# Kernel tuning notes

Measured on AMD Instinct MI355X. Metric: run time of the kernel, lower is better.

The kernel has to match this reference:

```python
import jax, jax.numpy as jnp
from jax import lax
import numpy as np
import math

B, T, D = 4, 4096, 1024
K, H = 128, 8
KH = K // H
KER = 4
M = 4 * D  # mlp hidden


def _ln(x, g, b):
    m = jnp.mean(x, axis=-1, keepdims=True)
    v = jnp.var(x, axis=-1, keepdims=True)
    return (x - m) / jnp.sqrt(v + 1e-5) * g + b


def setup_inputs() -> dict:
    key = jax.random.key(0)
    ks = jax.random.split(key, 20)
    s = lambda i, shape, sc=0.02: jax.random.normal(ks[i], shape, dtype=jnp.float32) * sc
    inp = {}
    inp["x"] = jax.random.normal(ks[0], (B, T, D), dtype=jnp.float32)
    inp["prev_eig"] = jax.random.normal(ks[1], (B, T, 2 * K), dtype=jnp.float32)
    inp["in_proj_w"] = s(2, (2 * K, D))
    inp["conv_w"] = s(3, (2 * K, 1, KER), 0.3)          # depthwise Conv1d weight
    inp["conv_b"] = s(4, (2 * K,), 0.02)
    inp["mem_gate"] = jnp.float32(-3.0)
    inp["mem_proj_w"] = jnp.eye(2 * K, dtype=jnp.float32) + s(5, (2 * K, 2 * K), 0.02)
    # log_decay uniform in [center-1, center+0.5], center = -2 + 1.5*(1/5)
    center = -2.0 + 1.5 * (1.0 / 5.0)
    inp["log_decay"] = jax.random.uniform(ks[6], (K,), dtype=jnp.float32, minval=center - 1.0, maxval=center + 0.5)
    inp["frequency"] = jnp.linspace(0.0, 2.0 * math.pi * (1.0 - 1.0 / K), K, dtype=jnp.float32)
    inp["coupling"] = jnp.eye(KH, dtype=jnp.float32)[None] + 0.01 * jax.random.normal(ks[7], (H, KH, KH), dtype=jnp.float32) / math.sqrt(KH)
    inp["out_proj_w"] = s(8, (D, 2 * K))
    inp["gate_w"] = s(9, (D, D))
    inp["gate_b"] = jnp.full((D,), -2.0, dtype=jnp.float32)
    inp["mlp_w1"] = s(10, (M, D))
    inp["mlp_b1"] = jnp.zeros((M,), jnp.float32)
    inp["mlp_w2"] = s(11, (D, M))
    inp["mlp_b2"] = jnp.zeros((D,), jnp.float32)
    inp["n1_g"] = jnp.ones((D,), jnp.float32)
    inp["n1_b"] = jnp.zeros((D,), jnp.float32)
    inp["n2_g"] = jnp.ones((D,), jnp.float32)
    inp["n2_b"] = jnp.zeros((D,), jnp.float32)
    return inp


def reference(x, prev_eig, in_proj_w, conv_w, conv_b, mem_gate, mem_proj_w,
              log_decay, frequency, coupling, out_proj_w, gate_w, gate_b,
              mlp_w1, mlp_b1, mlp_w2, mlp_b2, n1_g, n1_b, n2_g, n2_b):
    Bn, Tn, Dn = x.shape
    xn = _ln(x, n1_g, n1_b)
    beta = xn @ in_proj_w.T                                   # [B,T,2K]
    # depthwise causal conv: torch pad=ker-1 both sides then [:, :, :T] == left-pad ker-1 + valid
    ker = conv_w.shape[-1]
    bp = jnp.pad(beta, ((0, 0), (ker - 1, 0), (0, 0))).transpose(0, 2, 1)  # [B,2K,T+ker-1]
    beta = lax.conv_general_dilated(bp, conv_w, (1,), 'VALID',
                                    feature_group_count=conv_w.shape[0],
                                    dimension_numbers=('NCH', 'OIH', 'NCH'))
    beta = jax.nn.silu(beta.transpose(0, 2, 1) + conv_b)       # [B,T,2K]
    br, bi = jnp.split(beta, 2, axis=-1)                       # [B,T,K] each
    # memory injection (has_memory: layer_idx > 0)
    mg = jax.nn.sigmoid(mem_gate)
    pr, pi = jnp.split(prev_eig @ mem_proj_w.T, 2, axis=-1)
    br = br + mg * pr
    bi = bi + mg * pi
    # eigenstate evolution via zero-padded complex FFT convolution
    mag = jax.nn.sigmoid(log_decay)                            # [K]
    n = jnp.arange(Tn, dtype=x.dtype)
    mag_pow = mag[None, :] ** n[:, None]                       # [T,K]
    phase = n[:, None] * frequency[None, :]
    kern = mag_pow * (jnp.cos(phase) + 1j * jnp.sin(phase))    # complex [T,K]
    beta_c = br + 1j * bi
    Bf = jnp.fft.fft(jnp.pad(beta_c, ((0, 0), (0, Tn), (0, 0))), axis=1)  # [B,2T,K]
    Kf = jnp.fft.fft(jnp.pad(kern, ((0, Tn), (0, 0))), axis=0)            # [2T,K]
    c = jnp.fft.ifft(Bf * Kf[None], axis=1)[:, :Tn]
    cr, ci = c.real.astype(x.dtype), c.imag.astype(x.dtype)
    # per-head coupling, batched over heads
    Hh, Kh = coupling.shape[0], coupling.shape[1]
    cr = jnp.einsum('hjk,bthk->bthj', coupling, cr.reshape(Bn, Tn, Hh, Kh)).reshape(Bn, Tn, Hh * Kh)
    ci = jnp.einsum('hjk,bthk->bthj', coupling, ci.reshape(Bn, Tn, Hh, Kh)).reshape(Bn, Tn, Hh * Kh)
    eig = jnp.concatenate([cr, ci], axis=-1)                   # [B,T,2K]
    h = jax.nn.sigmoid(xn @ gate_w.T + gate_b) * (eig @ out_proj_w.T)
    x1 = x + h
    y = _ln(x1, n2_g, n2_b)
    x2 = x1 + jax.nn.silu(y @ mlp_w1.T + mlp_b1) @ mlp_w2.T + mlp_b2
    return (x2, eig)
```

## Files before the change

### kernel.cpp

```cpp
#include <hip/hip_runtime.h>
#include <hip/hip_bf16.h>
#include <math.h>

#define Bn 4
#define Tn 4096
#define Dn 1024
#define Kn 128
#define TWOK 256
#define Hn 8
#define Mmlp 4096
#define NROW (Bn * Tn)
#define TAPS 16

typedef __attribute__((ext_vector_type(8))) short bf16x8;
typedef __attribute__((ext_vector_type(4))) float floatx4;

__device__ __forceinline__ float sigmoidf_(float x) { return 1.f / (1.f + expf(-x)); }

__global__ __launch_bounds__(256) void f2bf_kernel(const float* __restrict__ in,
                                                   __hip_bfloat16* __restrict__ out,
                                                   int n) {
    const int i = (blockIdx.x * 256 + threadIdx.x) * 4;
    if (i >= n) return;
    const float4 v = *(const float4*)(in + i);
    out[i + 0] = __float2bfloat16(v.x);
    out[i + 1] = __float2bfloat16(v.y);
    out[i + 2] = __float2bfloat16(v.z);
    out[i + 3] = __float2bfloat16(v.w);
}

__global__ __launch_bounds__(256) void ln_kernel(const float* __restrict__ x,
                                                 const float* __restrict__ g,
                                                 const float* __restrict__ b,
                                                 __hip_bfloat16* __restrict__ out) {
    const int row = blockIdx.x;
    const float4* xr = (const float4*)(x + (size_t)row * Dn);
    float4 v = xr[threadIdx.x];
    float s = v.x + v.y + v.z + v.w;
    float ss = v.x * v.x + v.y * v.y + v.z * v.z + v.w * v.w;
    for (int off = 32; off; off >>= 1) {
        s += __shfl_down(s, off);
        ss += __shfl_down(ss, off);
    }
    __shared__ float rs[4], rss[4];
    const int wv = threadIdx.x >> 6, ln = threadIdx.x & 63;
    if (ln == 0) { rs[wv] = s; rss[wv] = ss; }
    __syncthreads();
    s = rs[0] + rs[1] + rs[2] + rs[3];
    ss = rss[0] + rss[1] + rss[2] + rss[3];
    const float mean = s * (1.f / Dn);
    const float var = ss * (1.f / Dn) - mean * mean;
    const float inv = rsqrtf(var + 1e-5f);
    const float4 gg = ((const float4*)g)[threadIdx.x];
    const float4 bb = ((const float4*)b)[threadIdx.x];
    __hip_bfloat16* op = out + (size_t)row * Dn + threadIdx.x * 4;
    op[0] = __float2bfloat16((v.x - mean) * inv * gg.x + bb.x);
    op[1] = __float2bfloat16((v.y - mean) * inv * gg.y + bb.y);
    op[2] = __float2bfloat16((v.z - mean) * inv * gg.z + bb.z);
    op[3] = __float2bfloat16((v.w - mean) * inv * gg.w + bb.w);
}

template <int EPI, typename CT>
__global__ __launch_bounds__(256, EPI == 5 ? 2 : 4)
void gemm_bf(const ushort* __restrict__ A,
             const ushort* __restrict__ B,
             CT* __restrict__ C,
             int M, int N, int Kd,
             const float* __restrict__ bias,
             const float* __restrict__ aux1,
             const __hip_bfloat16* __restrict__ aux2,
             const ushort* __restrict__ A2, const ushort* __restrict__ B2, int Kd2) {
    __shared__ ushort As[128 * 32];
    __shared__ ushort Bs[128 * 32];
    const int tid = threadIdx.x;
    const int nbx = gridDim.x;
    const int nblk = nbx * gridDim.y;
    int bid = blockIdx.y * nbx + blockIdx.x;
    if ((nblk & 7) == 0)
        bid = (bid & 7) * (nblk >> 3) + (bid >> 3);
    const int m0 = (bid / nbx) * 128, n0 = (bid % nbx) * 128;
    const int wave = tid >> 6, lane = tid & 63;
    const int wm = wave >> 1, wn = wave & 1;
    const int mlane = lane & 15, quad = lane >> 4;

    floatx4 acc[4][4] = {};

    {
        const ushort* Ap = A + (size_t)m0 * Kd;
        const ushort* Bp = B + (size_t)n0 * Kd;
        for (int k0 = 0; k0 < Kd; k0 += 32) {
#pragma unroll
            for (int q = 0; q < 2; ++q) {
                const int c = q * 256 + tid;
                const int row = c >> 2, kc = (c & 3) * 8;
                __builtin_amdgcn_global_load_lds(
                    (const __attribute__((address_space(1))) void*)(Ap + (size_t)row * Kd + k0 + kc),
                    (__attribute__((address_space(3))) void*)(As + c * 8), 16, 0, 0);
                __builtin_amdgcn_global_load_lds(
                    (const __attribute__((address_space(1))) void*)(Bp + (size_t)row * Kd + k0 + kc),
                    (__attribute__((address_space(3))) void*)(Bs + c * 8), 16, 0, 0);
            }
            __syncthreads();
            bf16x8 af[4], bfr[4];
#pragma unroll
            for (int t = 0; t < 4; ++t) {
                af[t]  = *(const bf16x8*)&As[(wm * 64 + t * 16 + mlane) * 32 + quad * 8];
                bfr[t] = *(const bf16x8*)&Bs[(wn * 64 + t * 16 + mlane) * 32 + quad * 8];
            }
#pragma unroll
            for (int i = 0; i < 4; ++i)
#pragma unroll
                for (int j = 0; j < 4; ++j)
                    acc[i][j] = __builtin_amdgcn_mfma_f32_16x16x32_bf16(af[i], bfr[j], acc[i][j], 0, 0, 0);
            __syncthreads();
        }
    }

    floatx4 acc2[EPI == 5 ? 4 : 1][EPI == 5 ? 4 : 1] = {};
    if constexpr (EPI == 5) {
        const ushort* Ap = A2 + (size_t)m0 * Kd2;
        const ushort* Bp = B2 + (size_t)n0 * Kd2;
        for (int k0 = 0; k0 < Kd2; k0 += 32) {
#pragma unroll
            for (int q = 0; q < 2; ++q) {
                const int c = q * 256 + tid;
                const int row = c >> 2, kc = (c & 3) * 8;
                __builtin_amdgcn_global_load_lds(
                    (const __attribute__((address_space(1))) void*)(Ap + (size_t)row * Kd2 + k0 + kc),
                    (__attribute__((address_space(3))) void*)(As + c * 8), 16, 0, 0);
                __builtin_amdgcn_global_load_lds(
                    (const __attribute__((address_space(1))) void*)(Bp + (size_t)row * Kd2 + k0 + kc),
                    (__attribute__((address_space(3))) void*)(Bs + c * 8), 16, 0, 0);
            }
            __syncthreads();
            bf16x8 af[4], bfr[4];
#pragma unroll
            for (int t = 0; t < 4; ++t) {
                af[t]  = *(const bf16x8*)&As[(wm * 64 + t * 16 + mlane) * 32 + quad * 8];
                bfr[t] = *(const bf16x8*)&Bs[(wn * 64 + t * 16 + mlane) * 32 + quad * 8];
            }
#pragma unroll
            for (int i = 0; i < 4; ++i)
#pragma unroll
                for (int j = 0; j < 4; ++j)
                    acc2[i][j] = __builtin_amdgcn_mfma_f32_16x16x32_bf16(af[i], bfr[j], acc2[i][j], 0, 0, 0);
            __syncthreads();
        }
    }

    float s_pre = 0.f;
    if constexpr (EPI == 1) s_pre = sigmoidf_(bias[0]);

    const int cbase = n0 + wn * 64 + mlane;
#pragma unroll
    for (int i = 0; i < 4; ++i) {
#pragma unroll
        for (int r = 0; r < 4; ++r) {
            const int row = m0 + wm * 64 + i * 16 + quad * 4 + r;
            const size_t ro = (size_t)row * N;
#pragma unroll
            for (int j = 0; j < 4; ++j) {
                const int col = cbase + j * 16;
                const float a = acc[i][j][r];
                float o;
                if constexpr (EPI == 0) {
                    o = a;
                } else if constexpr (EPI == 1) {
                    o = s_pre * a;
                } else if constexpr (EPI == 2) {
                    o = aux1[ro + col] + sigmoidf_(a + bias[col]) * __bfloat162float(aux2[ro + col]);
                } else if constexpr (EPI == 3) {
                    const float t = a + bias[col];
                    o = t * sigmoidf_(t);
                } else if constexpr (EPI == 4) {
                    o = a + bias[col] + aux1[ro + col];
                } else {
                    o = aux1[ro + col] + sigmoidf_(a + bias[col]) * acc2[i][j][r];
                }
                if constexpr (__is_same(CT, float)) C[ro + col] = o;
                else                                C[ro + col] = __float2bfloat16(o);
            }
        }
    }
}

template <int EPI, typename CT>
__global__ __launch_bounds__(512, 2)
void gemm256(const ushort* __restrict__ A, const ushort* __restrict__ B,
             CT* __restrict__ C, int N, int Kd,
             const float* __restrict__ bias, const float* __restrict__ aux1,
             const __hip_bfloat16* __restrict__ aux2) {
    __shared__ ushort As[2][256 * 64];
    __shared__ ushort Bs[2][256 * 64];
    const int tid = threadIdx.x;
    const int nbx = gridDim.x;
    const int nblk = nbx * gridDim.y;
    int bid = blockIdx.y * nbx + blockIdx.x;
    if ((nblk & 7) == 0)
        bid = (bid & 7) * (nblk >> 3) + (bid >> 3);
    const int m0 = (bid / nbx) * 256, n0 = (bid % nbx) * 256;
    const int wave = tid >> 6, lane = tid & 63;
    const int wm = wave >> 2, wn = wave & 3;
    const int mlane = lane & 15, quad = lane >> 4;
    const int NT = Kd >> 6;

    const int srow = tid >> 3;
    const size_t sgoff = (size_t)srow * Kd + (size_t)(((tid & 7) ^ (srow & 7)) << 3);

    auto stA = [&](int s, int half) {
        const int r0 = half * 64;
        const ushort* g = A + (size_t)(m0 + r0) * Kd + (s << 6) + sgoff;
        ushort* l = &As[s & 1][(r0 << 6) + (tid << 3)];
        __builtin_amdgcn_global_load_lds(
            (const __attribute__((address_space(1))) void*)g,
            (__attribute__((address_space(3))) void*)l, 16, 0, 0);
        __builtin_amdgcn_global_load_lds(
            (const __attribute__((address_space(1))) void*)(g + (size_t)128 * Kd),
            (__attribute__((address_space(3))) void*)(l + (128 << 6)), 16, 0, 0);
    };
    auto stB = [&](int s, int half) {
        const int r0 = half * 128;
        const ushort* g = B + (size_t)(n0 + r0) * Kd + (s << 6) + sgoff;
        ushort* l = &Bs[s & 1][(r0 << 6) + (tid << 3)];
        __builtin_amdgcn_global_load_lds(
            (const __attribute__((address_space(1))) void*)g,
            (__attribute__((address_space(3))) void*)l, 16, 0, 0);
        __builtin_amdgcn_global_load_lds(
            (const __attribute__((address_space(1))) void*)(g + (size_t)64 * Kd),
            (__attribute__((address_space(3))) void*)(l + (64 << 6)), 16, 0, 0);
    };

    floatx4 acc[8][4] = {};
    bf16x8 a[4][2], b[4][2];

    const int ar = (wm * 128 + mlane) << 6;
    const int br = (wn * 64 + mlane) << 6;
    const int o0 = (quad ^ (mlane & 7)) << 3;
    const int o1 = ((4 + quad) ^ (mlane & 7)) << 3;

#define MFMA16(MB, NB)                                                           \
    __builtin_amdgcn_s_setprio(1);                                               \
    _Pragma("unroll")                                                            \
    for (int m_ = 0; m_ < 4; ++m_) {                                             \
        _Pragma("unroll")                                                        \
        for (int n_ = 0; n_ < 2; ++n_) {                                         \
            acc[MB + m_][NB + n_] = __builtin_amdgcn_mfma_f32_16x16x32_bf16(     \
                a[m_][0], b[NB + n_][0], acc[MB + m_][NB + n_], 0, 0, 0);        \
            acc[MB + m_][NB + n_] = __builtin_amdgcn_mfma_f32_16x16x32_bf16(     \
                a[m_][1], b[NB + n_][1], acc[MB + m_][NB + n_], 0, 0, 0);        \
        }                                                                        \
    }                                                                            \
    __builtin_amdgcn_s_setprio(0);

    stA(0, 0); stA(0, 1); stB(0, 0); stB(0, 1);
    __builtin_amdgcn_sched_barrier(0);
    stA(1, 0); stB(1, 0); stA(1, 1);
    asm volatile("s_waitcnt vmcnt(6)" ::: "memory");
    __builtin_amdgcn_s_barrier();

    for (int t = 0; t < NT; ++t) {
        const ushort* Ab = &As[t & 1][0];
        const ushort* Bb = &Bs[t & 1][0];
#pragma unroll
        for (int m = 0; m < 4; ++m) {
            a[m][0] = *(const bf16x8*)(Ab + ar + m * 1024 + o0);
            a[m][1] = *(const bf16x8*)(Ab + ar + m * 1024 + o1);
        }
#pragma unroll
        for (int n = 0; n < 2; ++n) {
            b[n][0] = *(const bf16x8*)(Bb + br + n * 1024 + o0);
            b[n][1] = *(const bf16x8*)(Bb + br + n * 1024 + o1);
        }
        if (t + 1 < NT) stB(t + 1, 1);
        __builtin_amdgcn_s_barrier();
        asm volatile("s_waitcnt lgkmcnt(0)" ::: "memory");
        __builtin_amdgcn_sched_barrier(0);
        MFMA16(0, 0)
        __builtin_amdgcn_s_barrier();
#pragma unroll
        for (int n = 0; n < 2; ++n) {
            b[2 + n][0] = *(const bf16x8*)(Bb + br + (2 + n) * 1024 + o0);
            b[2 + n][1] = *(const bf16x8*)(Bb + br + (2 + n) * 1024 + o1);
        }
        if (t + 2 < NT) stA(t + 2, 0);
        __builtin_amdgcn_s_barrier();
        asm volatile("s_waitcnt lgkmcnt(0)" ::: "memory");
        __builtin_amdgcn_sched_barrier(0);
        MFMA16(0, 2)
        __builtin_amdgcn_s_barrier();
#pragma unroll
        for (int m = 0; m < 4; ++m) {
            a[m][0] = *(const bf16x8*)(Ab + ar + (4 + m) * 1024 + o0);
            a[m][1] = *(const bf16x8*)(Ab + ar + (4 + m) * 1024 + o1);
        }
        if (t + 2 < NT) stB(t + 2, 0);
        __builtin_amdgcn_s_barrier();
        asm volatile("s_waitcnt lgkmcnt(0)" ::: "memory");
        __builtin_amdgcn_sched_barrier(0);
        MFMA16(4, 0)
        __builtin_amdgcn_s_barrier();
        if (t + 2 < NT) stA(t + 2, 1);
        MFMA16(4, 2)
        if (t + 2 < NT) {
            asm volatile("s_waitcnt vmcnt(6)" ::: "memory");
        } else if (t + 1 < NT) {
            asm volatile("s_waitcnt vmcnt(0)" ::: "memory");
        }
        if (t + 1 < NT) __builtin_amdgcn_s_barrier();
    }
#undef MFMA16

    const int cbase = n0 + wn * 64 + mlane;
#pragma unroll
    for (int m = 0; m < 8; ++m) {
#pragma unroll
        for (int r = 0; r < 4; ++r) {
            const int row = m0 + wm * 128 + m * 16 + quad * 4 + r;
            const size_t ro = (size_t)row * N;
#pragma unroll
            for (int n = 0; n < 4; ++n) {
                const int col = cbase + n * 16;
                const float av = acc[m][n][r];
                float o;
                if constexpr (EPI == 0) {
                    o = av;
                } else if constexpr (EPI == 2) {
                    o = aux1[ro + col] + sigmoidf_(av + bias[col]) * __bfloat162float(aux2[ro + col]);
                } else if constexpr (EPI == 3) {
                    const float tt = av + bias[col];
                    o = tt * sigmoidf_(tt);
                } else {
                    o = av + bias[col] + aux1[ro + col];
                }
                if constexpr (__is_same(CT, float)) C[ro + col] = o;
                else                                C[ro + col] = __float2bfloat16(o);
            }
        }
    }
}

#define TCH 256
#define BROWS (TCH + TAPS + 2)
#define UROWS (TCH + TAPS - 1)

__global__ __launch_bounds__(256) void cfc_kernel(const float* __restrict__ beta,
                                                  const float* __restrict__ mgp,
                                                  const float* __restrict__ conv_w,
                                                  const float* __restrict__ conv_b,
                                                  const float* __restrict__ log_decay,
                                                  const float* __restrict__ freq,
                                                  const float* __restrict__ coup,
                                                  float* __restrict__ eig,
                                                  __hip_bfloat16* __restrict__ eig_bf) {
    const int b = blockIdx.z, h = blockIdx.y, t0 = blockIdx.x * TCH;
    const int tid = threadIdx.x;

    __shared__ float sbeta[BROWS * 32];
    __shared__ float su[UROWS * 33];
    __shared__ float str[16 * TAPS], sti[16 * TAPS];
    __shared__ float scoup[16 * 16];
    __shared__ float scw[32 * 4], scb[32];

    auto chan = [&](int cg) { return (cg < 16) ? (h * 16 + cg) : (128 + h * 16 + cg - 16); };

    for (int idx = tid; idx < BROWS * 32; idx += 256) {
        const int r = idx >> 5, cg = idx & 31;
        const int t = t0 - (TAPS + 2) + r;
        sbeta[idx] = (t >= 0) ? beta[((size_t)b * Tn + t) * TWOK + chan(cg)] : 0.f;
    }
    for (int idx = tid; idx < UROWS * 32; idx += 256) {
        const int r = idx >> 5, cg = idx & 31;
        const int t = t0 - (TAPS - 1) + r;
        su[r * 33 + cg] = (t >= 0) ? mgp[((size_t)b * Tn + t) * TWOK + chan(cg)] : 0.f;
    }
    if (tid < 128) scw[tid] = conv_w[chan(tid >> 2) * 4 + (tid & 3)];
    else if (tid < 160) scb[tid - 128] = conv_b[chan(tid - 128)];
    scoup[tid] = coup[h * 256 + tid];
    {
        const int k = tid >> 4, d = tid & (TAPS - 1);
        const float mag = sigmoidf_(log_decay[h * 16 + k]);
        const float f = freq[h * 16 + k];
        const float p = powf(mag, (float)d);
        str[k * TAPS + d] = p * cosf(d * f);
        sti[k * TAPS + d] = p * sinf(d * f);
    }
    __syncthreads();

    for (int idx = tid; idx < UROWS * 32; idx += 256) {
        const int r = idx >> 5, cg = idx & 31;
        const int rb = r + 3;
        float v = sbeta[(rb - 3) * 32 + cg] * scw[cg * 4 + 0] +
                  sbeta[(rb - 2) * 32 + cg] * scw[cg * 4 + 1] +
                  sbeta[(rb - 1) * 32 + cg] * scw[cg * 4 + 2] +
                  sbeta[(rb - 0) * 32 + cg] * scw[cg * 4 + 3] + scb[cg];
        v = v * sigmoidf_(v);
        su[r * 33 + cg] += v;
    }
    __syncthreads();

    const int ru = tid + (TAPS - 1);
    float orr[16], oii[16];
#pragma unroll
    for (int j = 0; j < 16; ++j) { orr[j] = 0.f; oii[j] = 0.f; }
#pragma unroll 4
    for (int k = 0; k < 16; ++k) {
        float accr = 0.f, acci = 0.f;
#pragma unroll
        for (int d = 0; d < TAPS; ++d) {
            const float ur = su[(ru - d) * 33 + k];
            const float ui = su[(ru - d) * 33 + 16 + k];
            const float lr = str[k * TAPS + d], li = sti[k * TAPS + d];
            accr += lr * ur - li * ui;
            acci += lr * ui + li * ur;
        }
#pragma unroll
        for (int j = 0; j < 16; ++j) {
            orr[j] += scoup[j * 16 + k] * accr;
            oii[j] += scoup[j * 16 + k] * acci;
        }
    }
    const size_t base = ((size_t)b * Tn + t0 + tid) * TWOK + h * 16;
    float4* er = (float4*)(eig + base);
    float4* ei = (float4*)(eig + base + Kn);
#pragma unroll
    for (int q = 0; q < 4; ++q) {
        er[q] = make_float4(orr[4 * q], orr[4 * q + 1], orr[4 * q + 2], orr[4 * q + 3]);
        ei[q] = make_float4(oii[4 * q], oii[4 * q + 1], oii[4 * q + 2], oii[4 * q + 3]);
    }
#pragma unroll
    for (int j = 0; j < 16; ++j) {
        eig_bf[base + j] = __float2bfloat16(orr[j]);
        eig_bf[base + Kn + j] = __float2bfloat16(oii[j]);
    }
}

extern "C" void kernel_launch(void* const* d_in, const int* in_sizes, int n_in,
                              void* d_out, int out_size, void* d_ws, size_t ws_size,
                              hipStream_t stream) {
    const float* x          = (const float*)d_in[0];
    const float* prev_eig   = (const float*)d_in[1];
    const float* in_proj_w  = (const float*)d_in[2];
    const float* conv_w     = (const float*)d_in[3];
    const float* conv_b     = (const float*)d_in[4];
    const float* mem_gate   = (const float*)d_in[5];
    const float* mem_proj_w = (const float*)d_in[6];
    const float* log_decay  = (const float*)d_in[7];
    const float* frequency  = (const float*)d_in[8];
    const float* coupling   = (const float*)d_in[9];
    const float* out_proj_w = (const float*)d_in[10];
    const float* gate_w     = (const float*)d_in[11];
    const float* gate_b     = (const float*)d_in[12];
    const float* mlp_w1     = (const float*)d_in[13];
    const float* mlp_b1     = (const float*)d_in[14];
    const float* mlp_w2     = (const float*)d_in[15];
    const float* mlp_b2     = (const float*)d_in[16];
    const float* n1_g       = (const float*)d_in[17];
    const float* n1_b       = (const float*)d_in[18];
    const float* n2_g       = (const float*)d_in[19];
    const float* n2_b       = (const float*)d_in[20];

    float* out = (float*)d_out;
    float* eig = out + (size_t)NROW * Dn;

    char* wsb = (char*)d_ws;
    const size_t MB = 1 << 20;
    const bool bigws = ws_size >= 252 * MB;

    float* x1    = (float*)(wsb + 0);
    float* beta  = (float*)(wsb + 0);
    float* mgp   = (float*)(wsb + 16 * MB);
    __hip_bfloat16 *h1, *eig_bf, *peig_bf, *xn_bf, *y_bf, *w1_bf, *w2_bf,
                   *gate_bf, *inpj_bf, *outpj_bf, *mempj_bf;
    if (bigws) {
        h1       = (__hip_bfloat16*)(wsb + 64 * MB);
        xn_bf    = (__hip_bfloat16*)(wsb + 192 * MB);
        y_bf     = (__hip_bfloat16*)(wsb + 192 * MB);
        w1_bf    = (__hip_bfloat16*)(wsb + 224 * MB);
        w2_bf    = (__hip_bfloat16*)(wsb + 232 * MB);
        gate_bf  = (__hip_bfloat16*)(wsb + 240 * MB);
        inpj_bf  = (__hip_bfloat16*)(wsb + 242 * MB);
        outpj_bf = (__hip_bfloat16*)(wsb + 242 * MB + 512 * 1024);
        mempj_bf = (__hip_bfloat16*)(wsb + 243 * MB);
        peig_bf  = (__hip_bfloat16*)(wsb + 244 * MB);
        eig_bf   = (__hip_bfloat16*)(wsb + 244 * MB);
    } else {
        h1       = (__hip_bfloat16*)(wsb + 64 * MB);
        eig_bf   = (__hip_bfloat16*)(wsb + 96 * MB);
        peig_bf  = (__hip_bfloat16*)(wsb + 104 * MB);
        xn_bf    = (__hip_bfloat16*)(wsb + 128 * MB);
        y_bf     = (__hip_bfloat16*)(wsb + 160 * MB);
        w1_bf    = (__hip_bfloat16*)(wsb + 192 * MB);
        w2_bf    = (__hip_bfloat16*)(wsb + 200 * MB);
        gate_bf  = (__hip_bfloat16*)(wsb + 208 * MB);
        inpj_bf  = (__hip_bfloat16*)(wsb + 210 * MB);
        outpj_bf = (__hip_bfloat16*)(wsb + 210 * MB + 512 * 1024);
        mempj_bf = (__hip_bfloat16*)(wsb + 211 * MB);
    }

    auto cvt = [&](const float* src, __hip_bfloat16* dst, int n) {
        f2bf_kernel<<<dim3((n / 4 + 255) / 256), dim3(256), 0, stream>>>(src, dst, n);
    };
    cvt(in_proj_w,  inpj_bf,  TWOK * Dn);
    cvt(mem_proj_w, mempj_bf, TWOK * TWOK);
    cvt(out_proj_w, outpj_bf, Dn * TWOK);
    cvt(gate_w,     gate_bf,  Dn * Dn);
    cvt(mlp_w1,     w1_bf,    Mmlp * Dn);
    cvt(mlp_w2,     w2_bf,    Dn * Mmlp);
    cvt(prev_eig,   peig_bf,  NROW * TWOK);

    ln_kernel<<<dim3(NROW), dim3(256), 0, stream>>>(x, n1_g, n1_b, xn_bf);
    gemm_bf<0, float><<<dim3(2, 128), dim3(256), 0, stream>>>(
        (const ushort*)xn_bf, (const ushort*)inpj_bf, beta, NROW, TWOK, Dn,
        nullptr, nullptr, nullptr, nullptr, nullptr, 0);
    gemm_bf<1, float><<<dim3(2, 128), dim3(256), 0, stream>>>(
        (const ushort*)peig_bf, (const ushort*)mempj_bf, mgp, NROW, TWOK, TWOK,
        mem_gate, nullptr, nullptr, nullptr, nullptr, 0);
    cfc_kernel<<<dim3(Tn / TCH, Hn, Bn), dim3(256), 0, stream>>>(
        beta, mgp, conv_w, conv_b, log_decay, frequency, coupling, eig, eig_bf);
    gemm_bf<5, float><<<dim3(8, 128), dim3(256), 0, stream>>>(
        (const ushort*)xn_bf, (const ushort*)gate_bf, x1, NROW, Dn, Dn,
        gate_b, x, nullptr, (const ushort*)eig_bf, (const ushort*)outpj_bf, TWOK);
    ln_kernel<<<dim3(NROW), dim3(256), 0, stream>>>(x1, n2_g, n2_b, y_bf);
    if (bigws) {
        gemm256<3, __hip_bfloat16><<<dim3(16, 64), dim3(512), 0, stream>>>(
            (const ushort*)y_bf, (const ushort*)w1_bf, h1, Mmlp, Dn,
            mlp_b1, nullptr, nullptr);
        gemm256<4, float><<<dim3(4, 64), dim3(512), 0, stream>>>(
            (const ushort*)h1, (const ushort*)w2_bf, out, Dn, Mmlp,
            mlp_b2, x1, nullptr);
    } else {
        for (int ck = 0; ck < 2; ++ck) {
            const size_t roff = (size_t)ck * 8192 * Dn;
            gemm256<3, __hip_bfloat16><<<dim3(16, 32), dim3(512), 0, stream>>>(
                (const ushort*)(y_bf + roff), (const ushort*)w1_bf, h1, Mmlp, Dn,
                mlp_b1, nullptr, nullptr);
            gemm256<4, float><<<dim3(4, 32), dim3(512), 0, stream>>>(
                (const ushort*)h1, (const ushort*)w2_bf, out + roff, Dn, Mmlp,
                mlp_b2, x1 + roff, nullptr);
        }
    }
}
```

Measured before the change: 723.5 us.

## Split gate GEMM into two gemm256 launches, add XCD-grouped tiling, relax LDS waits

The fused gate/out_proj GEMM (128x128 tiles, dual accumulators) is replaced by two 256x256 gemm256 launches. The first writes eig@out_proj^T as bf16 into h1, and the second applies the sigmoid gate and residual using it. gemm256 gains a column-group XCD tile mapping for L2 locality, reorders its B/A fragment loads, and drops the explicit lgkmcnt(0) waits so the compiler places them. sigmoid now uses fast __expf. The split adds an extra bf16 intermediate round trip, and the looser wait ordering depends on the compiler inserting correct waits.

After: 726.1 us. No clear change (+0.3%).

```diff
diff --git a/kernel.cpp b/kernel.cpp
--- a/kernel.cpp
+++ b/kernel.cpp
@@ -15,7 +15,7 @@
 typedef __attribute__((ext_vector_type(8))) short bf16x8;
 typedef __attribute__((ext_vector_type(4))) float floatx4;
 
-__device__ __forceinline__ float sigmoidf_(float x) { return 1.f / (1.f + expf(-x)); }
+__device__ __forceinline__ float sigmoidf_(float x) { return 1.f / (1.f + __expf(-x)); }
 
 __global__ __launch_bounds__(256) void f2bf_kernel(const float* __restrict__ in,
                                                    __hip_bfloat16* __restrict__ out,
@@ -61,15 +61,12 @@
 }
 
 template <int EPI, typename CT>
-__global__ __launch_bounds__(256, EPI == 5 ? 2 : 4)
+__global__ __launch_bounds__(256, 4)
 void gemm_bf(const ushort* __restrict__ A,
              const ushort* __restrict__ B,
              CT* __restrict__ C,
              int M, int N, int Kd,
-             const float* __restrict__ bias,
-             const float* __restrict__ aux1,
-             const __hip_bfloat16* __restrict__ aux2,
-             const ushort* __restrict__ A2, const ushort* __restrict__ B2, int Kd2) {
+             const float* __restrict__ bias) {
     __shared__ ushort As[128 * 32];
     __shared__ ushort Bs[128 * 32];
     const int tid = threadIdx.x;
@@ -116,38 +113,6 @@
         }
     }
 
-    floatx4 acc2[EPI == 5 ? 4 : 1][EPI == 5 ? 4 : 1] = {};
-    if constexpr (EPI == 5) {
-        const ushort* Ap = A2 + (size_t)m0 * Kd2;
-        const ushort* Bp = B2 + (size_t)n0 * Kd2;
-        for (int k0 = 0; k0 < Kd2; k0 += 32) {
-#pragma unroll
-            for (int q = 0; q < 2; ++q) {
-                const int c = q * 256 + tid;
-                const int row = c >> 2, kc = (c & 3) * 8;
-                __builtin_amdgcn_global_load_lds(
-                    (const __attribute__((address_space(1))) void*)(Ap + (size_t)row * Kd2 + k0 + kc),
-                    (__attribute__((address_space(3))) void*)(As + c * 8), 16, 0, 0);
-                __builtin_amdgcn_global_load_lds(
-                    (const __attribute__((address_space(1))) void*)(Bp + (size_t)row * Kd2 + k0 + kc),
-                    (__attribute__((address_space(3))) void*)(Bs + c * 8), 16, 0, 0);
-            }
-            __syncthreads();
-            bf16x8 af[4], bfr[4];
-#pragma unroll
-            for (int t = 0; t < 4; ++t) {
-                af[t]  = *(const bf16x8*)&As[(wm * 64 + t * 16 + mlane) * 32 + quad * 8];
-                bfr[t] = *(const bf16x8*)&Bs[(wn * 64 + t * 16 + mlane) * 32 + quad * 8];
-            }
-#pragma unroll
-            for (int i = 0; i < 4; ++i)
-#pragma unroll
-                for (int j = 0; j < 4; ++j)
-                    acc2[i][j] = __builtin_amdgcn_mfma_f32_16x16x32_bf16(af[i], bfr[j], acc2[i][j], 0, 0, 0);
-            __syncthreads();
-        }
-    }
-
     float s_pre = 0.f;
     if constexpr (EPI == 1) s_pre = sigmoidf_(bias[0]);
 
@@ -163,20 +128,8 @@
                 const int col = cbase + j * 16;
                 const float a = acc[i][j][r];
                 float o;
-                if constexpr (EPI == 0) {
-                    o = a;
-                } else if constexpr (EPI == 1) {
-                    o = s_pre * a;
-                } else if constexpr (EPI == 2) {
-                    o = aux1[ro + col] + sigmoidf_(a + bias[col]) * __bfloat162float(aux2[ro + col]);
-                } else if constexpr (EPI == 3) {
-                    const float t = a + bias[col];
-                    o = t * sigmoidf_(t);
-                } else if constexpr (EPI == 4) {
-                    o = a + bias[col] + aux1[ro + col];
-                } else {
-                    o = aux1[ro + col] + sigmoidf_(a + bias[col]) * acc2[i][j][r];
-                }
+                if constexpr (EPI == 0) o = a;
+                else                    o = s_pre * a;
                 if constexpr (__is_same(CT, float)) C[ro + col] = o;
                 else                                C[ro + col] = __float2bfloat16(o);
             }
@@ -189,27 +142,40 @@
 void gemm256(const ushort* __restrict__ A, const ushort* __restrict__ B,
              CT* __restrict__ C, int N, int Kd,
              const float* __restrict__ bias, const float* __restrict__ aux1,
-             const __hip_bfloat16* __restrict__ aux2) {
+             const __hip_bfloat16* __restrict__ aux2, int cg) {
     __shared__ ushort As[2][256 * 64];
     __shared__ ushort Bs[2][256 * 64];
     const int tid = threadIdx.x;
     const int nbx = gridDim.x;
     const int nblk = nbx * gridDim.y;
+    const int nrows = nblk / nbx;
     int bid = blockIdx.y * nbx + blockIdx.x;
-    if ((nblk & 7) == 0)
-        bid = (bid & 7) * (nblk >> 3) + (bid >> 3);
-    const int m0 = (bid / nbx) * 256, n0 = (bid % nbx) * 256;
+    int mt, ntile;
+    if ((nblk & 7) == 0 && cg > 0 && nbx % cg == 0 && nrows % (8 / cg) == 0) {
+        const int xcd = bid & 7, i = bid >> 3;
+        const int cPerG = nbx / cg;
+        const int rPerG = nrows / (8 / cg);
+        const int rg = xcd / cg, cgi = xcd % cg;
+        mt = rg * rPerG + i / cPerG;
+        ntile = cgi * cPerG + i % cPerG;
+    } else {
+        mt = bid / nbx; ntile = bid % nbx;
+    }
+    const int m0 = mt * 256, n0 = ntile * 256;
     const int wave = tid >> 6, lane = tid & 63;
     const int wm = wave >> 2, wn = wave & 3;
     const int mlane = lane & 15, quad = lane >> 4;
     const int NT = Kd >> 6;
 
     const int srow = tid >> 3;
-    const size_t sgoff = (size_t)srow * Kd + (size_t)(((tid & 7) ^ (srow & 7)) << 3);
+    const ushort* Abase = A + (size_t)m0 * Kd + (size_t)srow * Kd +
+                          (size_t)(((tid & 7) ^ (srow & 7)) << 3);
+    const ushort* Bbase = B + (size_t)n0 * Kd + (size_t)srow * Kd +
+                          (size_t)(((tid & 7) ^ (srow & 7)) << 3);
 
     auto stA = [&](int s, int half) {
         const int r0 = half * 64;
-        const ushort* g = A + (size_t)(m0 + r0) * Kd + (s << 6) + sgoff;
+        const ushort* g = Abase + (size_t)r0 * Kd + (s << 6);
         ushort* l = &As[s & 1][(r0 << 6) + (tid << 3)];
         __builtin_amdgcn_global_load_lds(
             (const __attribute__((address_space(1))) void*)g,
@@ -220,7 +186,7 @@
     };
     auto stB = [&](int s, int half) {
         const int r0 = half * 128;
-        const ushort* g = B + (size_t)(n0 + r0) * Kd + (s << 6) + sgoff;
+        const ushort* g = Bbase + (size_t)r0 * Kd + (s << 6);
         ushort* l = &Bs[s & 1][(r0 << 6) + (tid << 3)];
         __builtin_amdgcn_global_load_lds(
             (const __attribute__((address_space(1))) void*)g,
@@ -262,20 +228,19 @@
         const ushort* Ab = &As[t & 1][0];
         const ushort* Bb = &Bs[t & 1][0];
 #pragma unroll
+        for (int n = 0; n < 2; ++n) {
+            b[n][0] = *(const bf16x8*)(Bb + br + n * 1024 + o0);
+            b[n][1] = *(const bf16x8*)(Bb + br + n * 1024 + o1);
+        }
+#pragma unroll
         for (int m = 0; m < 4; ++m) {
             a[m][0] = *(const bf16x8*)(Ab + ar + m * 1024 + o0);
             a[m][1] = *(const bf16x8*)(Ab + ar + m * 1024 + o1);
         }
-#pragma unroll
-        for (int n = 0; n < 2; ++n) {
-            b[n][0] = *(const bf16x8*)(Bb + br + n * 1024 + o0);
-            b[n][1] = *(const bf16x8*)(Bb + br + n * 1024 + o1);
-        }
         if (t + 1 < NT) stB(t + 1, 1);
         __builtin_amdgcn_s_barrier();
-        asm volatile("s_waitcnt lgkmcnt(0)" ::: "memory");
+        MFMA16(0, 0)
         __builtin_amdgcn_sched_barrier(0);
-        MFMA16(0, 0)
         __builtin_amdgcn_s_barrier();
 #pragma unroll
         for (int n = 0; n < 2; ++n) {
@@ -284,9 +249,8 @@
         }
         if (t + 2 < NT) stA(t + 2, 0);
         __builtin_amdgcn_s_barrier();
-        asm volatile("s_waitcnt lgkmcnt(0)" ::: "memory");
+        MFMA16(0, 2)
         __builtin_amdgcn_sched_barrier(0);
-        MFMA16(0, 2)
         __builtin_amdgcn_s_barrier();
 #pragma unroll
         for (int m = 0; m < 4; ++m) {
@@ -295,9 +259,8 @@
         }
         if (t + 2 < NT) stB(t + 2, 0);
         __builtin_amdgcn_s_barrier();
-        asm volatile("s_waitcnt lgkmcnt(0)" ::: "memory");
+        MFMA16(4, 0)
         __builtin_amdgcn_sched_barrier(0);
-        MFMA16(4, 0)
         __builtin_amdgcn_s_barrier();
         if (t + 2 < NT) stA(t + 2, 1);
         MFMA16(4, 2)
@@ -306,6 +269,7 @@
         } else if (t + 1 < NT) {
             asm volatile("s_waitcnt vmcnt(0)" ::: "memory");
         }
+        __builtin_amdgcn_sched_barrier(0);
         if (t + 1 < NT) __builtin_amdgcn_s_barrier();
     }
 #undef MFMA16
@@ -510,33 +474,34 @@
 
     ln_kernel<<<dim3(NROW), dim3(256), 0, stream>>>(x, n1_g, n1_b, xn_bf);
     gemm_bf<0, float><<<dim3(2, 128), dim3(256), 0, stream>>>(
-        (const ushort*)xn_bf, (const ushort*)inpj_bf, beta, NROW, TWOK, Dn,
-        nullptr, nullptr, nullptr, nullptr, nullptr, 0);
+        (const ushort*)xn_bf, (const ushort*)inpj_bf, beta, NROW, TWOK, Dn, nullptr);
     gemm_bf<1, float><<<dim3(2, 128), dim3(256), 0, stream>>>(
-        (const ushort*)peig_bf, (const ushort*)mempj_bf, mgp, NROW, TWOK, TWOK,
-        mem_gate, nullptr, nullptr, nullptr, nullptr, 0);
+        (const ushort*)peig_bf, (const ushort*)mempj_bf, mgp, NROW, TWOK, TWOK, mem_gate);
     cfc_kernel<<<dim3(Tn / TCH, Hn, Bn), dim3(256), 0, stream>>>(
         beta, mgp, conv_w, conv_b, log_decay, frequency, coupling, eig, eig_bf);
-    gemm_bf<5, float><<<dim3(8, 128), dim3(256), 0, stream>>>(
-        (const ushort*)xn_bf, (const ushort*)gate_bf, x1, NROW, Dn, Dn,
-        gate_b, x, nullptr, (const ushort*)eig_bf, (const ushort*)outpj_bf, TWOK);
+    gemm256<0, __hip_bfloat16><<<dim3(4, 64), dim3(512), 0, stream>>>(
+        (const ushort*)eig_bf, (const ushort*)outpj_bf, h1, Dn, TWOK,
+        nullptr, nullptr, nullptr, 2);
+    gemm256<2, float><<<dim3(4, 64), dim3(512), 0, stream>>>(
+        (const ushort*)xn_bf, (const ushort*)gate_bf, x1, Dn, Dn,
+        gate_b, x, h1, 2);
     ln_kernel<<<dim3(NROW), dim3(256), 0, stream>>>(x1, n2_g, n2_b, y_bf);
     if (bigws) {
         gemm256<3, __hip_bfloat16><<<dim3(16, 64), dim3(512), 0, stream>>>(
             (const ushort*)y_bf, (const ushort*)w1_bf, h1, Mmlp, Dn,
-            mlp_b1, nullptr, nullptr);
+            mlp_b1, nullptr, nullptr, 2);
         gemm256<4, float><<<dim3(4, 64), dim3(512), 0, stream>>>(
             (const ushort*)h1, (const ushort*)w2_bf, out, Dn, Mmlp,
-            mlp_b2, x1, nullptr);
+            mlp_b2, x1, nullptr, 2);
     } else {
         for (int ck = 0; ck < 2; ++ck) {
             const size_t roff = (size_t)ck * 8192 * Dn;
             gemm256<3, __hip_bfloat16><<<dim3(16, 32), dim3(512), 0, stream>>>(
                 (const ushort*)(y_bf + roff), (const ushort*)w1_bf, h1, Mmlp, Dn,
-                mlp_b1, nullptr, nullptr);
+                mlp_b1, nullptr, nullptr, 2);
             gemm256<4, float><<<dim3(4, 32), dim3(512), 0, stream>>>(
                 (const ushort*)h1, (const ushort*)w2_bf, out + roff, Dn, Mmlp,
-                mlp_b2, x1 + roff, nullptr);
+                mlp_b2, x1 + roff, nullptr, 2);
         }
     }
 }
```
